# Performance work log

Measured on AMD Instinct MI355X. Metric: run time of the kernel, lower is better.

## Reference

```python
import jax, jax.numpy as jnp
import numpy as np

# ---- static config (matches init_kwargs) ----
N, E = 8192, 262144
IN_CH, MP_CH, HID, K = 128, 512, 256, 10
EPS, DELTA = 1e-3, 0.311
TV_COEFF, BAL_COEFF = 0.785, 0.514


def setup_inputs() -> dict:
    key = jax.random.key(0)
    ks = jax.random.split(key, 16)

    def p(k, shape):
        fan_in = shape[0] if len(shape) > 1 else shape[0]
        return (jax.random.normal(k, shape, jnp.float32) / np.sqrt(fan_in)).astype(jnp.float32)

    return {
        "x": jax.random.normal(ks[0], (N, IN_CH), jnp.float32),
        "edge_index": jax.random.randint(ks[1], (2, E), 0, N, jnp.int32),
        "edge_weight": jax.random.uniform(ks[2], (E,), jnp.float32),
        # GTVConv layer 1 / 2 (Linear weight + bias)
        "W1": p(ks[3], (IN_CH, MP_CH)), "b1": jnp.zeros((MP_CH,), jnp.float32),
        "W2": p(ks[4], (MP_CH, MP_CH)), "b2": jnp.zeros((MP_CH,), jnp.float32),
        # pooling MLP [512 -> 256 -> K], relu, no norm
        "Wm1": p(ks[5], (MP_CH, HID)), "bm1": jnp.zeros((HID,), jnp.float32),
        "Wm2": p(ks[6], (HID, K)), "bm2": jnp.zeros((K,), jnp.float32),
    }


def _gtv_conv(x, src, dst, w, W, b):
    """GTVConv: out = elu( h - delta*(D_G h - Gamma h) + b ),
    gamma_ij = w_ij / max(||h_i - h_j||_1, eps), h = x @ W."""
    h = x @ W                                   # [N, C]
    diff = jnp.sum(jnp.abs(h[src] - h[dst]), axis=-1)   # [E]
    gamma = w / jnp.maximum(diff, EPS)                  # [E]
    deg = jnp.zeros(h.shape[0], h.dtype).at[dst].add(gamma)          # [N]
    agg = jnp.zeros_like(h).at[dst].add(gamma[:, None] * h[src])     # Gamma @ h
    out = h - DELTA * (deg[:, None] * h - agg) + b
    return jax.nn.elu(out)


def reference(x, edge_index, edge_weight, W1, b1, W2, b2, Wm1, bm1, Wm2, bm2):
    src, dst = edge_index[0], edge_index[1]

    h = _gtv_conv(x, src, dst, edge_weight, W1, b1)
    h = _gtv_conv(h, src, dst, edge_weight, W2, b2)

    # pooling MLP -> cluster logits s
    s_logits = jax.nn.relu(h @ Wm1 + bm1) @ Wm2 + bm2   # [N, K]

    # dense adjacency (to_dense_adj: duplicate edges accumulate)
    adj = jnp.zeros((N, N), x.dtype).at[src, dst].add(edge_weight)

    s = jax.nn.softmax(s_logits, axis=-1)

    # total-variation loss: sum_ij a_ij * sum_k |s_ik - s_jk| / (2 * nnz(adj))
    tv = jnp.zeros((), x.dtype)
    for k in range(K):  # small fixed loop over clusters, avoids [N,N,K] tensor
        col = s[:, k]
        tv = tv + jnp.sum(adj * jnp.abs(col[:, None] - col[None, :]))
    n_edges = jax.lax.stop_gradient(jnp.count_nonzero(adj).astype(x.dtype))
    tv = tv / (2.0 * n_edges)

    # asymmetric-norm balance loss (AsymCheegerCut)
    idx = N // K + 1                         # rho-quantile index (static)
    quant = jnp.sort(s, axis=0)[N - idx]     # idx-th largest per cluster, [K]
    t = s - quant[None, :]
    asym = jnp.where(t >= 0, (K - 1) * t, -t)
    denom = float(N * (K - 1))
    bal = (denom - jnp.sum(asym)) / denom

    return s_logits, TV_COEFF * tv, BAL_COEFF * bal
```

## Files before the change

### kernel.cpp

```cpp
#include <hip/hip_runtime.h>

#define N_NODES 8192
#define N_EDGES 262144
#define IN_CH 128
#define MP_CH 512
#define HID 256
#define KCL 10
#define EPS_C 0.001f
#define DELTA_C 0.311f
#define TV_COEFF_C 0.785f
#define BAL_COEFF_C 0.514f
#define RANK1 7373
#define DBINS 80

typedef __bf16 bf16x8 __attribute__((ext_vector_type(8)));
typedef float f32x4 __attribute__((ext_vector_type(4)));
typedef unsigned short ushort8 __attribute__((ext_vector_type(8)));

__device__ __forceinline__ float bf2f(unsigned short h) {
  union { unsigned int u; float f; } c; c.u = ((unsigned int)h) << 16; return c.f;
}
__device__ __forceinline__ unsigned short f2bf(float f) {
  union { float f; unsigned int u; } c; c.f = f;
  unsigned int r = c.u + 0x7fffu + ((c.u >> 16) & 1u);
  return (unsigned short)(r >> 16);
}

__global__ void prep_kernel(const float* __restrict__ x, const float* __restrict__ W1,
                            const float* __restrict__ W2, const float* __restrict__ Wm1,
                            unsigned short* __restrict__ xb, unsigned short* __restrict__ W1bt,
                            unsigned short* __restrict__ W2bt, unsigned short* __restrict__ Wm1bt,
                            const int* __restrict__ dst, int* __restrict__ cnt) {
  int i = blockIdx.x * 256 + threadIdx.x;
  if (i < 1048576) { xb[i] = f2bf(x[i]); return; }
  i -= 1048576;
  if (i < 65536) { int n = i >> 7, k = i & 127; W1bt[i] = f2bf(W1[k * MP_CH + n]); return; }
  i -= 65536;
  if (i < 262144) { int n = i >> 9, k = i & 511; W2bt[i] = f2bf(W2[k * MP_CH + n]); return; }
  i -= 262144;
  if (i < 131072) { int n = i >> 9, k = i & 511; Wm1bt[i] = f2bf(Wm1[k * HID + n]); return; }
  i -= 131072;
  if (i < N_EDGES) atomicAdd(&cnt[dst[i]], 1);
}

__global__ __launch_bounds__(1024) void scan_kernel(const int* __restrict__ cnt,
                                                    int* __restrict__ offs,
                                                    int* __restrict__ cursor,
                                                    int* __restrict__ nodeorder) {
  __shared__ int ts[1024];
  __shared__ int dh[DBINS];
  int t = threadIdx.x;
  int v[8]; int s = 0;
#pragma unroll
  for (int j = 0; j < 8; ++j) { v[j] = cnt[t * 8 + j]; s += v[j]; }
  if (t < DBINS) dh[t] = 0;
  ts[t] = s; __syncthreads();
  for (int off = 1; off < 1024; off <<= 1) {
    int add = (t >= off) ? ts[t - off] : 0;
    __syncthreads();
    ts[t] += add;
    __syncthreads();
  }
  int base = ts[t] - s;
#pragma unroll
  for (int j = 0; j < 8; ++j) {
    offs[t * 8 + j] = base; cursor[t * 8 + j] = base; base += v[j];
    int key = v[j] < (DBINS - 1) ? v[j] : (DBINS - 1);
    atomicAdd(&dh[(DBINS - 1) - key], 1);
  }
  if (t == 1023) offs[N_NODES] = ts[1023];
  __syncthreads();
  if (t == 0) {
    int acc0 = 0;
    for (int b = 0; b < DBINS; ++b) { int c = dh[b]; dh[b] = acc0; acc0 += c; }
  }
  __syncthreads();
#pragma unroll
  for (int j = 0; j < 8; ++j) {
    int key = v[j] < (DBINS - 1) ? v[j] : (DBINS - 1);
    int pos = atomicAdd(&dh[(DBINS - 1) - key], 1);
    nodeorder[pos] = t * 8 + j;
  }
}

__global__ void fill_kernel(const int* __restrict__ src, const int* __restrict__ dst,
                            const float* __restrict__ ew, int* __restrict__ cursor,
                            int2* __restrict__ esw) {
  for (int e = blockIdx.x * blockDim.x + threadIdx.x; e < N_EDGES; e += gridDim.x * blockDim.x) {
    int p = atomicAdd(&cursor[dst[e]], 1);
    esw[p] = make_int2(src[e], __float_as_int(ew[e]));
  }
}

__global__ __launch_bounds__(256) void gemm_bt(
    const unsigned short* __restrict__ A, const unsigned short* __restrict__ BT,
    float* __restrict__ C, unsigned short* __restrict__ Cb,
    const float* __restrict__ bias, int N, int K, int epi) {
  __shared__ unsigned short lsm[2 * 128 * 32];
  unsigned short* lA = lsm;
  unsigned short* lB = lsm + 128 * 32;
  int lane = threadIdx.x & 63;
  int wv = threadIdx.x >> 6;
  int tm = blockIdx.y * 128, tn = blockIdx.x * 128;
  int wm = (wv >> 1) * 64, wn = (wv & 1) * 64;
  int rA = lane & 15, quad = lane >> 4;
  f32x4 acc[4][4];
#pragma unroll
  for (int i = 0; i < 4; ++i)
#pragma unroll
    for (int j = 0; j < 4; ++j) acc[i][j] = (f32x4){0.f, 0.f, 0.f, 0.f};

  int arow = wv * 32 + (lane >> 2);
  int acol = (lane & 3) * 8;

  for (int k0 = 0; k0 < K; k0 += 32) {
#pragma unroll
    for (int c = 0; c < 2; ++c) {
      const unsigned short* ga = A + (size_t)(tm + arow + c * 16) * K + k0 + acol;
      __builtin_amdgcn_global_load_lds(
          (const __attribute__((address_space(1))) unsigned int*)ga,
          (__attribute__((address_space(3))) unsigned int*)(lA + (wv * 32 + c * 16) * 32),
          16, 0, 0);
      const unsigned short* gb = BT + (size_t)(tn + arow + c * 16) * K + k0 + acol;
      __builtin_amdgcn_global_load_lds(
          (const __attribute__((address_space(1))) unsigned int*)gb,
          (__attribute__((address_space(3))) unsigned int*)(lB + (wv * 32 + c * 16) * 32),
          16, 0, 0);
    }
    __syncthreads();
    bf16x8 af[4], bfr[4];
#pragma unroll
    for (int i = 0; i < 4; ++i)
      af[i] = *(const bf16x8*)(lA + (wm + i * 16 + rA) * 32 + quad * 8);
#pragma unroll
    for (int j = 0; j < 4; ++j)
      bfr[j] = *(const bf16x8*)(lB + (wn + j * 16 + rA) * 32 + quad * 8);
#pragma unroll
    for (int i = 0; i < 4; ++i)
#pragma unroll
      for (int j = 0; j < 4; ++j)
        acc[i][j] = __builtin_amdgcn_mfma_f32_16x16x32_bf16(af[i], bfr[j], acc[i][j], 0, 0, 0);
    __syncthreads();
  }

  if (epi == 1) {
#pragma unroll
    for (int i = 0; i < 4; ++i)
#pragma unroll
      for (int j = 0; j < 4; ++j)
#pragma unroll
        for (int r = 0; r < 4; ++r) {
          int row = tm + wm + i * 16 + quad * 4 + r;
          int col = tn + wn + j * 16 + rA;
          float v = acc[i][j][r] + bias[col];
          C[(size_t)row * N + col] = fmaxf(v, 0.f);
        }
  } else {
    float* fbuf = (float*)lsm;
    int band = threadIdx.x >> 7;
    int rrow = (threadIdx.x >> 3) & 15;
    int cg = threadIdx.x & 7;
#pragma unroll
    for (int i = 0; i < 4; ++i) {
#pragma unroll
      for (int j = 0; j < 4; ++j)
#pragma unroll
        for (int r = 0; r < 4; ++r)
          fbuf[(wv >> 1) * (16 * 128) + (quad * 4 + r) * 128 + (wn + j * 16 + rA)] =
              acc[i][j][r];
      __syncthreads();
      const float* sr = fbuf + band * (16 * 128) + rrow * 128 + cg * 16;
      unsigned short ov[16];
#pragma unroll
      for (int c = 0; c < 16; ++c) ov[c] = f2bf(sr[c]);
      size_t base = (size_t)(tm + band * 64 + i * 16 + rrow) * N + tn + cg * 16;
      *(ushort8*)(Cb + base) = *(ushort8*)ov;
      *(ushort8*)(Cb + base + 8) = *(ushort8*)(ov + 8);
      __syncthreads();
    }
  }
}

__global__ __launch_bounds__(256, 8) void gtv_node(
    const unsigned short* __restrict__ hb, const float* __restrict__ bias,
    const int2* __restrict__ esw, const int* __restrict__ offs,
    const int* __restrict__ nodeorder, unsigned short* __restrict__ outb) {
  __shared__ float sacc[2][MP_CH];
  int lane = threadIdx.x & 63;
  int wv = threadIdx.x >> 6;
  int pair = wv >> 1;
  int half = wv & 1;
  int d = __builtin_amdgcn_readfirstlane(nodeorder[blockIdx.x * 2 + pair]);
  ushort8 hdv = ((const ushort8*)(hb + (size_t)d * MP_CH))[lane];
  float hd[8], acc[8];
#pragma unroll
  for (int j = 0; j < 8; ++j) { hd[j] = bf2f(hdv[j]); acc[j] = 0.f; }
  int n0 = offs[d], n1 = offs[d + 1];
  int mid = n0 + ((n1 - n0 + 1) >> 1);
  int e0 = half ? mid : n0;
  int e1 = half ? n1 : mid;
  int i = e0;
  for (; i + 1 < e1; i += 2) {
    int2 ma = esw[i], mb = esw[i + 1];
    float wa = __int_as_float(ma.y), wb = __int_as_float(mb.y);
    ushort8 va = ((const ushort8*)(hb + (size_t)ma.x * MP_CH))[lane];
    ushort8 vb = ((const ushort8*)(hb + (size_t)mb.x * MP_CH))[lane];
    float pa = 0.f, pb = 0.f;
#pragma unroll
    for (int j = 0; j < 8; ++j) {
      pa += fabsf(hd[j] - bf2f(va[j]));
      pb += fabsf(hd[j] - bf2f(vb[j]));
    }
#pragma unroll
    for (int m = 1; m < 64; m <<= 1) { pa += __shfl_xor(pa, m, 64); pb += __shfl_xor(pb, m, 64); }
    float ga = wa * __builtin_amdgcn_rcpf(fmaxf(pa, EPS_C));
    float gb = wb * __builtin_amdgcn_rcpf(fmaxf(pb, EPS_C));
#pragma unroll
    for (int j = 0; j < 8; ++j)
      acc[j] += ga * (hd[j] - bf2f(va[j])) + gb * (hd[j] - bf2f(vb[j]));
  }
  if (i < e1) {
    int2 m0 = esw[i];
    float w = __int_as_float(m0.y);
    ushort8 sv = ((const ushort8*)(hb + (size_t)m0.x * MP_CH))[lane];
    float part = 0.f;
#pragma unroll
    for (int j = 0; j < 8; ++j) part += fabsf(hd[j] - bf2f(sv[j]));
#pragma unroll
    for (int m = 1; m < 64; m <<= 1) part += __shfl_xor(part, m, 64);
    float g = w * __builtin_amdgcn_rcpf(fmaxf(part, EPS_C));
#pragma unroll
    for (int j = 0; j < 8; ++j) acc[j] += g * (hd[j] - bf2f(sv[j]));
  }
  if (half) {
#pragma unroll
    for (int j = 0; j < 8; ++j) sacc[pair][lane * 8 + j] = acc[j];
  }
  __syncthreads();
  if (!half) {
    const f32x4* br = (const f32x4*)(bias + lane * 8);
    f32x4 b0 = br[0], b1 = br[1];
    unsigned short ov[8];
#pragma unroll
    for (int j = 0; j < 8; ++j) {
      float tot = acc[j] + sacc[pair][lane * 8 + j];
      float bv = (j < 4) ? b0[j] : b1[j - 4];
      float o = hd[j] - DELTA_C * tot + bv;
      o = (o > 0.f) ? o : (expf(o) - 1.f);
      ov[j] = f2bf(o);
    }
    *((ushort8*)(outb + (size_t)d * MP_CH) + lane) = *(ushort8*)ov;
  }
}

__global__ __launch_bounds__(256) void gemm_small(
    const float* __restrict__ hm, const float* __restrict__ W,
    const float* __restrict__ b, float* __restrict__ out, float* __restrict__ s) {
  __shared__ float lw[HID * KCL];
  __shared__ float lb[KCL];
  for (int i = threadIdx.x; i < HID * KCL; i += 256) lw[i] = W[i];
  if (threadIdx.x < KCL) lb[threadIdx.x] = b[threadIdx.x];
  __syncthreads();
  int lane = threadIdx.x & 63, wv = threadIdx.x >> 6;
  int row = blockIdx.x * 4 + wv;
  f32x4 hv = *(const f32x4*)(hm + (size_t)row * HID + lane * 4);
  float p[KCL];
#pragma unroll
  for (int n = 0; n < KCL; ++n) {
    int k0 = lane * 4;
    p[n] = hv[0] * lw[(k0 + 0) * KCL + n] + hv[1] * lw[(k0 + 1) * KCL + n] +
           hv[2] * lw[(k0 + 2) * KCL + n] + hv[3] * lw[(k0 + 3) * KCL + n];
  }
#pragma unroll
  for (int n = 0; n < KCL; ++n)
#pragma unroll
    for (int m = 1; m < 64; m <<= 1) p[n] += __shfl_xor(p[n], m, 64);
  if (lane == 0) {
    float vv[KCL]; float mx = -1e30f;
#pragma unroll
    for (int n = 0; n < KCL; ++n) {
      vv[n] = p[n] + lb[n];
      out[(size_t)row * KCL + n] = vv[n];
      mx = fmaxf(mx, vv[n]);
    }
    float sum = 0.f;
#pragma unroll
    for (int n = 0; n < KCL; ++n) { vv[n] = expf(vv[n] - mx); sum += vv[n]; }
    float inv = 1.f / sum;
#pragma unroll
    for (int n = 0; n < KCL; ++n) s[(size_t)row * KCL + n] = vv[n] * inv;
  }
}

__global__ __launch_bounds__(1024) void tvquant_kernel(
    const int* __restrict__ src, const int* __restrict__ dst,
    const float* __restrict__ ew, const float* __restrict__ s,
    unsigned int* __restrict__ bitmap, float* __restrict__ scal) {
  __shared__ float fsh[16];
  __shared__ int wcnt[2][16];
  int t = threadIdx.x;
  int lane = t & 63, wv = t >> 6;
  if (blockIdx.x < 246) {
    float local = 0.f;
    for (int e = blockIdx.x * 1024 + t; e < N_EDGES; e += 246 * 1024) {
      int a = src[e], b = dst[e];
      float w = ew[e];
      const float* sa = s + (size_t)a * KCL;
      const float* sb = s + (size_t)b * KCL;
      float tv = 0.f;
#pragma unroll
      for (int k = 0; k < KCL; ++k) tv += fabsf(sa[k] - sb[k]);
      local += w * tv;
      if (w != 0.f) {
        unsigned int key = ((unsigned int)a << 13) | (unsigned int)b;
        atomicOr(&bitmap[key >> 5], 1u << (key & 31u));
      }
    }
#pragma unroll
    for (int m = 1; m < 64; m <<= 1) local += __shfl_xor(local, m, 64);
    if (lane == 0) fsh[wv] = local;
    __syncthreads();
    if (t == 0) {
      float tot = 0.f;
#pragma unroll
      for (int i2 = 0; i2 < 16; ++i2) tot += fsh[i2];
      atomicAdd(&scal[0], tot);
    }
  } else {
    int k = blockIdx.x - 246;
    unsigned int v[8];
#pragma unroll
    for (int j = 0; j < 8; ++j)
      v[j] = __float_as_uint(s[(size_t)(t + j * 1024) * KCL + k]);
    unsigned int lo = 0u, hi = 0x3F800000u;
    int p = 0;
    while (lo < hi) {
      unsigned int mid = (lo + hi) >> 1;
      int c = 0;
#pragma unroll
      for (int j = 0; j < 8; ++j) c += (v[j] <= mid) ? 1 : 0;
#pragma unroll
      for (int m = 1; m < 64; m <<= 1) c += __shfl_xor(c, m, 64);
      if (lane == 0) wcnt[p][wv] = c;
      __syncthreads();
      int tot = 0;
#pragma unroll
      for (int i2 = 0; i2 < 16; ++i2) tot += wcnt[p][i2];
      if (tot >= RANK1) hi = mid; else lo = mid + 1;
      p ^= 1;
    }
    float q = __uint_as_float(lo);
    float local = 0.f;
#pragma unroll
    for (int j = 0; j < 8; ++j) {
      float tt = __uint_as_float(v[j]) - q;
      local += (tt >= 0.f) ? 9.f * tt : -tt;
    }
#pragma unroll
    for (int m = 1; m < 64; m <<= 1) local += __shfl_xor(local, m, 64);
    if (lane == 0) fsh[wv] = local;
    __syncthreads();
    if (t == 0) {
      float tot = 0.f;
#pragma unroll
      for (int i2 = 0; i2 < 16; ++i2) tot += fsh[i2];
      atomicAdd(&scal[1], tot);
    }
  }
}

__global__ __launch_bounds__(1024) void popcfin_kernel(const unsigned int* __restrict__ bm,
                                                       float* __restrict__ scal,
                                                       float* __restrict__ out) {
  __shared__ int ish[16];
  int t = threadIdx.x;
  int lane = t & 63, wv = t >> 6;
  int local = 0;
  for (int i = blockIdx.x * 1024 + t; i < (1 << 21); i += 256 * 1024)
    local += __popc(bm[i]);
#pragma unroll
  for (int m = 1; m < 64; m <<= 1) local += __shfl_xor(local, m, 64);
  if (lane == 0) ish[wv] = local;
  __syncthreads();
  if (t == 0) {
    int tot = 0;
#pragma unroll
    for (int i2 = 0; i2 < 16; ++i2) tot += ish[i2];
    atomicAdd((int*)(scal + 2), tot);
    __threadfence();
    int d = atomicAdd((int*)(scal + 3), 1);
    if (d == 255) {
      float tv = scal[0], asym = scal[1];
      float nedges = (float)(*(int*)(scal + 2));
      out[N_NODES * KCL] = TV_COEFF_C * (tv / (2.f * nedges));
      out[N_NODES * KCL + 1] = BAL_COEFF_C * ((73728.f - asym) / 73728.f);
    }
  }
}

#define OFF_BM     ((size_t)0)
#define OFF_CNT    ((size_t)8388608)
#define OFF_SCAL   ((size_t)8421376)
#define OFF_OFFS   ((size_t)8421888)
#define OFF_CURSOR ((size_t)8454912)
#define OFF_NORD   ((size_t)8487936)
#define OFF_HB     ((size_t)16777216)
#define OFF_OUTB   ((size_t)25165824)
#define OFF_HM     ((size_t)33554432)
#define OFF_XB     ((size_t)41943040)
#define OFF_W1BT   ((size_t)44040192)
#define OFF_W2BT   ((size_t)44171264)
#define OFF_WM1BT  ((size_t)44695552)
#define OFF_S      ((size_t)44957696)

extern "C" void kernel_launch(void* const* d_in, const int* in_sizes, int n_in,
                              void* d_out, int out_size, void* d_ws, size_t ws_size,
                              hipStream_t stream) {
  const float* x   = (const float*)d_in[0];
  const int*   ei  = (const int*)d_in[1];
  const float* ew  = (const float*)d_in[2];
  const float* W1  = (const float*)d_in[3];
  const float* b1  = (const float*)d_in[4];
  const float* W2  = (const float*)d_in[5];
  const float* b2  = (const float*)d_in[6];
  const float* Wm1 = (const float*)d_in[7];
  const float* bm1 = (const float*)d_in[8];
  const float* Wm2 = (const float*)d_in[9];
  const float* bm2 = (const float*)d_in[10];
  float* out = (float*)d_out;

  char* ws = (char*)d_ws;
  unsigned int*   bitmap = (unsigned int*)(ws + OFF_BM);
  int*            cnt    = (int*)(ws + OFF_CNT);
  float*          scal   = (float*)(ws + OFF_SCAL);
  int*            offs   = (int*)(ws + OFF_OFFS);
  int*            cursor = (int*)(ws + OFF_CURSOR);
  int*            nord   = (int*)(ws + OFF_NORD);
  unsigned short* hb     = (unsigned short*)(ws + OFF_HB);
  unsigned short* outb   = (unsigned short*)(ws + OFF_OUTB);
  float*          hm     = (float*)(ws + OFF_HM);
  int2*           esw    = (int2*)(ws + OFF_HM);
  unsigned short* xb     = (unsigned short*)(ws + OFF_XB);
  unsigned short* W1bt   = (unsigned short*)(ws + OFF_W1BT);
  unsigned short* W2bt   = (unsigned short*)(ws + OFF_W2BT);
  unsigned short* Wm1bt  = (unsigned short*)(ws + OFF_WM1BT);
  float*          s      = (float*)(ws + OFF_S);

  const int* srcA = ei;
  const int* dstA = ei + N_EDGES;

  hipMemsetAsync(ws, 0, 8421632, stream);

  prep_kernel<<<6912, 256, 0, stream>>>(x, W1, W2, Wm1, xb, W1bt, W2bt, Wm1bt, dstA, cnt);
  scan_kernel<<<1, 1024, 0, stream>>>(cnt, offs, cursor, nord);
  fill_kernel<<<1024, 256, 0, stream>>>(srcA, dstA, ew, cursor, esw);

  gemm_bt<<<dim3(MP_CH / 128, N_NODES / 128), 256, 0, stream>>>(
      xb, W1bt, nullptr, hb, nullptr, MP_CH, IN_CH, 2);
  gtv_node<<<N_NODES / 2, 256, 0, stream>>>(hb, b1, esw, offs, nord, outb);
  gemm_bt<<<dim3(MP_CH / 128, N_NODES / 128), 256, 0, stream>>>(
      outb, W2bt, nullptr, hb, nullptr, MP_CH, MP_CH, 2);
  gtv_node<<<N_NODES / 2, 256, 0, stream>>>(hb, b2, esw, offs, nord, outb);
  gemm_bt<<<dim3(HID / 128, N_NODES / 128), 256, 0, stream>>>(
      outb, Wm1bt, hm, nullptr, bm1, HID, MP_CH, 1);
  gemm_small<<<N_NODES / 4, 256, 0, stream>>>(hm, Wm2, bm2, out, s);

  tvquant_kernel<<<256, 1024, 0, stream>>>(srcA, dstA, ew, s, bitmap, scal);
  popcfin_kernel<<<256, 1024, 0, stream>>>(bitmap, scal, out);
}
```

Measured before the change: 259.4 us.

## Switch intermediate storage from bf16 to fp16 and use packed half math in GTV aggregation

```diff
diff --git a/kernel.cpp b/kernel.cpp
--- a/kernel.cpp
+++ b/kernel.cpp
@@ -13,32 +13,32 @@
 #define RANK1 7373
 #define DBINS 80
 
-typedef __bf16 bf16x8 __attribute__((ext_vector_type(8)));
+typedef _Float16 f16x8 __attribute__((ext_vector_type(8)));
+typedef _Float16 f16x2 __attribute__((ext_vector_type(2)));
 typedef float f32x4 __attribute__((ext_vector_type(4)));
-typedef unsigned short ushort8 __attribute__((ext_vector_type(8)));
-
-__device__ __forceinline__ float bf2f(unsigned short h) {
-  union { unsigned int u; float f; } c; c.u = ((unsigned int)h) << 16; return c.f;
-}
-__device__ __forceinline__ unsigned short f2bf(float f) {
-  union { float f; unsigned int u; } c; c.f = f;
-  unsigned int r = c.u + 0x7fffu + ((c.u >> 16) & 1u);
-  return (unsigned short)(r >> 16);
+
+__device__ __forceinline__ f16x2 habs2(f16x2 a) {
+  unsigned int u;
+  __builtin_memcpy(&u, &a, 4);
+  u &= 0x7FFF7FFFu;
+  f16x2 r;
+  __builtin_memcpy(&r, &u, 4);
+  return r;
 }
 
 __global__ void prep_kernel(const float* __restrict__ x, const float* __restrict__ W1,
                             const float* __restrict__ W2, const float* __restrict__ Wm1,
-                            unsigned short* __restrict__ xb, unsigned short* __restrict__ W1bt,
-                            unsigned short* __restrict__ W2bt, unsigned short* __restrict__ Wm1bt,
+                            _Float16* __restrict__ xb, _Float16* __restrict__ W1bt,
+                            _Float16* __restrict__ W2bt, _Float16* __restrict__ Wm1bt,
                             const int* __restrict__ dst, int* __restrict__ cnt) {
   int i = blockIdx.x * 256 + threadIdx.x;
-  if (i < 1048576) { xb[i] = f2bf(x[i]); return; }
+  if (i < 1048576) { xb[i] = (_Float16)x[i]; return; }
   i -= 1048576;
-  if (i < 65536) { int n = i >> 7, k = i & 127; W1bt[i] = f2bf(W1[k * MP_CH + n]); return; }
+  if (i < 65536) { int n = i >> 7, k = i & 127; W1bt[i] = (_Float16)W1[k * MP_CH + n]; return; }
   i -= 65536;
-  if (i < 262144) { int n = i >> 9, k = i & 511; W2bt[i] = f2bf(W2[k * MP_CH + n]); return; }
+  if (i < 262144) { int n = i >> 9, k = i & 511; W2bt[i] = (_Float16)W2[k * MP_CH + n]; return; }
   i -= 262144;
-  if (i < 131072) { int n = i >> 9, k = i & 511; Wm1bt[i] = f2bf(Wm1[k * HID + n]); return; }
+  if (i < 131072) { int n = i >> 9, k = i & 511; Wm1bt[i] = (_Float16)Wm1[k * HID + n]; return; }
   i -= 131072;
   if (i < N_EDGES) atomicAdd(&cnt[dst[i]], 1);
 }
@@ -93,12 +93,12 @@
 }
 
 __global__ __launch_bounds__(256) void gemm_bt(
-    const unsigned short* __restrict__ A, const unsigned short* __restrict__ BT,
-    float* __restrict__ C, unsigned short* __restrict__ Cb,
+    const _Float16* __restrict__ A, const _Float16* __restrict__ BT,
+    float* __restrict__ C, _Float16* __restrict__ Cb,
     const float* __restrict__ bias, int N, int K, int epi) {
-  __shared__ unsigned short lsm[2 * 128 * 32];
-  unsigned short* lA = lsm;
-  unsigned short* lB = lsm + 128 * 32;
+  __shared__ _Float16 lsm[2 * 128 * 32];
+  _Float16* lA = lsm;
+  _Float16* lB = lsm + 128 * 32;
   int lane = threadIdx.x & 63;
   int wv = threadIdx.x >> 6;
   int tm = blockIdx.y * 128, tn = blockIdx.x * 128;
@@ -116,30 +116,30 @@
   for (int k0 = 0; k0 < K; k0 += 32) {
 #pragma unroll
     for (int c = 0; c < 2; ++c) {
-      const unsigned short* ga = A + (size_t)(tm + arow + c * 16) * K + k0 + acol;
+      const _Float16* ga = A + (size_t)(tm + arow + c * 16) * K + k0 + acol;
       __builtin_amdgcn_global_load_lds(
           (const __attribute__((address_space(1))) unsigned int*)ga,
           (__attribute__((address_space(3))) unsigned int*)(lA + (wv * 32 + c * 16) * 32),
           16, 0, 0);
-      const unsigned short* gb = BT + (size_t)(tn + arow + c * 16) * K + k0 + acol;
+      const _Float16* gb = BT + (size_t)(tn + arow + c * 16) * K + k0 + acol;
       __builtin_amdgcn_global_load_lds(
           (const __attribute__((address_space(1))) unsigned int*)gb,
           (__attribute__((address_space(3))) unsigned int*)(lB + (wv * 32 + c * 16) * 32),
           16, 0, 0);
     }
     __syncthreads();
-    bf16x8 af[4], bfr[4];
+    f16x8 af[4], bfr[4];
 #pragma unroll
     for (int i = 0; i < 4; ++i)
-      af[i] = *(const bf16x8*)(lA + (wm + i * 16 + rA) * 32 + quad * 8);
+      af[i] = *(const f16x8*)(lA + (wm + i * 16 + rA) * 32 + quad * 8);
 #pragma unroll
     for (int j = 0; j < 4; ++j)
-      bfr[j] = *(const bf16x8*)(lB + (wn + j * 16 + rA) * 32 + quad * 8);
+      bfr[j] = *(const f16x8*)(lB + (wn + j * 16 + rA) * 32 + quad * 8);
 #pragma unroll
     for (int i = 0; i < 4; ++i)
 #pragma unroll
       for (int j = 0; j < 4; ++j)
-        acc[i][j] = __builtin_amdgcn_mfma_f32_16x16x32_bf16(af[i], bfr[j], acc[i][j], 0, 0, 0);
+        acc[i][j] = __builtin_amdgcn_mfma_f32_16x16x32_f16(af[i], bfr[j], acc[i][j], 0, 0, 0);
     __syncthreads();
   }
 
@@ -170,31 +170,35 @@
               acc[i][j][r];
       __syncthreads();
       const float* sr = fbuf + band * (16 * 128) + rrow * 128 + cg * 16;
-      unsigned short ov[16];
-#pragma unroll
-      for (int c = 0; c < 16; ++c) ov[c] = f2bf(sr[c]);
+      f16x8 o1, o2;
+#pragma unroll
+      for (int c = 0; c < 8; ++c) { o1[c] = (_Float16)sr[c]; o2[c] = (_Float16)sr[c + 8]; }
       size_t base = (size_t)(tm + band * 64 + i * 16 + rrow) * N + tn + cg * 16;
-      *(ushort8*)(Cb + base) = *(ushort8*)ov;
-      *(ushort8*)(Cb + base + 8) = *(ushort8*)(ov + 8);
+      *(f16x8*)(Cb + base) = o1;
+      *(f16x8*)(Cb + base + 8) = o2;
       __syncthreads();
     }
   }
 }
 
 __global__ __launch_bounds__(256, 8) void gtv_node(
-    const unsigned short* __restrict__ hb, const float* __restrict__ bias,
+    const _Float16* __restrict__ hb, const float* __restrict__ bias,
     const int2* __restrict__ esw, const int* __restrict__ offs,
-    const int* __restrict__ nodeorder, unsigned short* __restrict__ outb) {
+    const int* __restrict__ nodeorder, _Float16* __restrict__ outb) {
   __shared__ float sacc[2][MP_CH];
+  const f16x2 one2 = {(_Float16)1.0f, (_Float16)1.0f};
   int lane = threadIdx.x & 63;
   int wv = threadIdx.x >> 6;
   int pair = wv >> 1;
   int half = wv & 1;
   int d = __builtin_amdgcn_readfirstlane(nodeorder[blockIdx.x * 2 + pair]);
-  ushort8 hdv = ((const ushort8*)(hb + (size_t)d * MP_CH))[lane];
-  float hd[8], acc[8];
-#pragma unroll
-  for (int j = 0; j < 8; ++j) { hd[j] = bf2f(hdv[j]); acc[j] = 0.f; }
+  f16x8 hdv = ((const f16x8*)(hb + (size_t)d * MP_CH))[lane];
+  f16x2 hd2[4], acc2[4];
+#pragma unroll
+  for (int p = 0; p < 4; ++p) {
+    hd2[p] = (f16x2){hdv[2 * p], hdv[2 * p + 1]};
+    acc2[p] = (f16x2){(_Float16)0.f, (_Float16)0.f};
+  }
   int n0 = offs[d], n1 = offs[d + 1];
   int mid = n0 + ((n1 - n0 + 1) >> 1);
   int e0 = half ? mid : n0;
@@ -203,53 +207,71 @@
   for (; i + 1 < e1; i += 2) {
     int2 ma = esw[i], mb = esw[i + 1];
     float wa = __int_as_float(ma.y), wb = __int_as_float(mb.y);
-    ushort8 va = ((const ushort8*)(hb + (size_t)ma.x * MP_CH))[lane];
-    ushort8 vb = ((const ushort8*)(hb + (size_t)mb.x * MP_CH))[lane];
+    f16x8 va = ((const f16x8*)(hb + (size_t)ma.x * MP_CH))[lane];
+    f16x8 vb = ((const f16x8*)(hb + (size_t)mb.x * MP_CH))[lane];
+    f16x2 da[4], db[4];
     float pa = 0.f, pb = 0.f;
 #pragma unroll
-    for (int j = 0; j < 8; ++j) {
-      pa += fabsf(hd[j] - bf2f(va[j]));
-      pb += fabsf(hd[j] - bf2f(vb[j]));
+    for (int p = 0; p < 4; ++p) {
+      f16x2 av = (f16x2){va[2 * p], va[2 * p + 1]};
+      f16x2 bv = (f16x2){vb[2 * p], vb[2 * p + 1]};
+      da[p] = hd2[p] - av;
+      db[p] = hd2[p] - bv;
+      pa = __builtin_amdgcn_fdot2(habs2(da[p]), one2, pa, false);
+      pb = __builtin_amdgcn_fdot2(habs2(db[p]), one2, pb, false);
     }
 #pragma unroll
     for (int m = 1; m < 64; m <<= 1) { pa += __shfl_xor(pa, m, 64); pb += __shfl_xor(pb, m, 64); }
     float ga = wa * __builtin_amdgcn_rcpf(fmaxf(pa, EPS_C));
     float gb = wb * __builtin_amdgcn_rcpf(fmaxf(pb, EPS_C));
-#pragma unroll
-    for (int j = 0; j < 8; ++j)
-      acc[j] += ga * (hd[j] - bf2f(va[j])) + gb * (hd[j] - bf2f(vb[j]));
+    f16x2 ga2 = {(_Float16)ga, (_Float16)ga};
+    f16x2 gb2 = {(_Float16)gb, (_Float16)gb};
+#pragma unroll
+    for (int p = 0; p < 4; ++p) {
+      acc2[p] += ga2 * da[p];
+      acc2[p] += gb2 * db[p];
+    }
   }
   if (i < e1) {
     int2 m0 = esw[i];
     float w = __int_as_float(m0.y);
-    ushort8 sv = ((const ushort8*)(hb + (size_t)m0.x * MP_CH))[lane];
+    f16x8 sv = ((const f16x8*)(hb + (size_t)m0.x * MP_CH))[lane];
+    f16x2 ds[4];
     float part = 0.f;
 #pragma unroll
-    for (int j = 0; j < 8; ++j) part += fabsf(hd[j] - bf2f(sv[j]));
+    for (int p = 0; p < 4; ++p) {
+      f16x2 svp = (f16x2){sv[2 * p], sv[2 * p + 1]};
+      ds[p] = hd2[p] - svp;
+      part = __builtin_amdgcn_fdot2(habs2(ds[p]), one2, part, false);
+    }
 #pragma unroll
     for (int m = 1; m < 64; m <<= 1) part += __shfl_xor(part, m, 64);
     float g = w * __builtin_amdgcn_rcpf(fmaxf(part, EPS_C));
-#pragma unroll
-    for (int j = 0; j < 8; ++j) acc[j] += g * (hd[j] - bf2f(sv[j]));
+    f16x2 g2 = {(_Float16)g, (_Float16)g};
+#pragma unroll
+    for (int p = 0; p < 4; ++p) acc2[p] += g2 * ds[p];
   }
   if (half) {
 #pragma unroll
-    for (int j = 0; j < 8; ++j) sacc[pair][lane * 8 + j] = acc[j];
+    for (int p = 0; p < 4; ++p) {
+      sacc[pair][lane * 8 + 2 * p] = (float)acc2[p][0];
+      sacc[pair][lane * 8 + 2 * p + 1] = (float)acc2[p][1];
+    }
   }
   __syncthreads();
   if (!half) {
     const f32x4* br = (const f32x4*)(bias + lane * 8);
     f32x4 b0 = br[0], b1 = br[1];
-    unsigned short ov[8];
+    f16x8 ov;
 #pragma unroll
     for (int j = 0; j < 8; ++j) {
-      float tot = acc[j] + sacc[pair][lane * 8 + j];
+      float aj = (float)acc2[j >> 1][j & 1] + sacc[pair][lane * 8 + j];
       float bv = (j < 4) ? b0[j] : b1[j - 4];
-      float o = hd[j] - DELTA_C * tot + bv;
+      float o = (float)hdv[j] - DELTA_C * aj + bv;
       o = (o > 0.f) ? o : (expf(o) - 1.f);
-      ov[j] = f2bf(o);
-    }
-    *((ushort8*)(outb + (size_t)d * MP_CH) + lane) = *(ushort8*)ov;
+      ov[j] = (_Float16)o;
+    }
+    ((f16x8*)(outb + (size_t)d * MP_CH))[lane] = ov;
   }
 }
 
@@ -430,21 +452,21 @@
   float* out = (float*)d_out;
 
   char* ws = (char*)d_ws;
-  unsigned int*   bitmap = (unsigned int*)(ws + OFF_BM);
-  int*            cnt    = (int*)(ws + OFF_CNT);
-  float*          scal   = (float*)(ws + OFF_SCAL);
-  int*            offs   = (int*)(ws + OFF_OFFS);
-  int*            cursor = (int*)(ws + OFF_CURSOR);
-  int*            nord   = (int*)(ws + OFF_NORD);
-  unsigned short* hb     = (unsigned short*)(ws + OFF_HB);
-  unsigned short* outb   = (unsigned short*)(ws + OFF_OUTB);
-  float*          hm     = (float*)(ws + OFF_HM);
-  int2*           esw    = (int2*)(ws + OFF_HM);
-  unsigned short* xb     = (unsigned short*)(ws + OFF_XB);
-  unsigned short* W1bt   = (unsigned short*)(ws + OFF_W1BT);
-  unsigned short* W2bt   = (unsigned short*)(ws + OFF_W2BT);
-  unsigned short* Wm1bt  = (unsigned short*)(ws + OFF_WM1BT);
-  float*          s      = (float*)(ws + OFF_S);
+  unsigned int* bitmap = (unsigned int*)(ws + OFF_BM);
+  int*          cnt    = (int*)(ws + OFF_CNT);
+  float*        scal   = (float*)(ws + OFF_SCAL);
+  int*          offs   = (int*)(ws + OFF_OFFS);
+  int*          cursor = (int*)(ws + OFF_CURSOR);
+  int*          nord   = (int*)(ws + OFF_NORD);
+  _Float16*     hb     = (_Float16*)(ws + OFF_HB);
+  _Float16*     outb   = (_Float16*)(ws + OFF_OUTB);
+  float*        hm     = (float*)(ws + OFF_HM);
+  int2*         esw    = (int2*)(ws + OFF_HM);
+  _Float16*     xb     = (_Float16*)(ws + OFF_XB);
+  _Float16*     W1bt   = (_Float16*)(ws + OFF_W1BT);
+  _Float16*     W2bt   = (_Float16*)(ws + OFF_W2BT);
+  _Float16*     Wm1bt  = (_Float16*)(ws + OFF_WM1BT);
+  float*        s      = (float*)(ws + OFF_S);
 
   const int* srcA = ei;
   const int* dstA = ei + N_EDGES;
```

Result: slower. 265.8 us (+2.5%).

## Count unique edges via CSR dedup instead of dense bitmap and popcount

Applied to the files above, without the earlier changes.

```diff
diff --git a/kernel.cpp b/kernel.cpp
--- a/kernel.cpp
+++ b/kernel.cpp
@@ -92,6 +92,29 @@
   }
 }
 
+__global__ __launch_bounds__(256) void dedup_kernel(const int2* __restrict__ esw,
+                                                    const int* __restrict__ offs,
+                                                    float* __restrict__ scal) {
+  __shared__ int wsum[4];
+  int lane = threadIdx.x & 63;
+  int wv = threadIdx.x >> 6;
+  int d = blockIdx.x * 4 + wv;
+  int e0 = offs[d], e1 = offs[d + 1];
+  int cnt = 0;
+  for (int p = e0 + lane; p < e1; p += 64) {
+    int sp = esw[p].x;
+    bool dup = false;
+    for (int q = e0; q < p; ++q) dup |= (esw[q].x == sp);
+    cnt += dup ? 0 : 1;
+  }
+#pragma unroll
+  for (int m = 1; m < 64; m <<= 1) cnt += __shfl_xor(cnt, m, 64);
+  if (lane == 0) wsum[wv] = cnt;
+  __syncthreads();
+  if (threadIdx.x == 0)
+    atomicAdd((int*)(scal + 2), wsum[0] + wsum[1] + wsum[2] + wsum[3]);
+}
+
 __global__ __launch_bounds__(256) void gemm_bt(
     const unsigned short* __restrict__ A, const unsigned short* __restrict__ BT,
     float* __restrict__ C, unsigned short* __restrict__ Cb,
@@ -295,7 +318,7 @@
 __global__ __launch_bounds__(1024) void tvquant_kernel(
     const int* __restrict__ src, const int* __restrict__ dst,
     const float* __restrict__ ew, const float* __restrict__ s,
-    unsigned int* __restrict__ bitmap, float* __restrict__ scal) {
+    float* __restrict__ scal, float* __restrict__ out) {
   __shared__ float fsh[16];
   __shared__ int wcnt[2][16];
   int t = threadIdx.x;
@@ -311,10 +334,6 @@
 #pragma unroll
       for (int k = 0; k < KCL; ++k) tv += fabsf(sa[k] - sb[k]);
       local += w * tv;
-      if (w != 0.f) {
-        unsigned int key = ((unsigned int)a << 13) | (unsigned int)b;
-        atomicOr(&bitmap[key >> 5], 1u << (key & 31u));
-      }
     }
 #pragma unroll
     for (int m = 1; m < 64; m <<= 1) local += __shfl_xor(local, m, 64);
@@ -367,29 +386,10 @@
       atomicAdd(&scal[1], tot);
     }
   }
-}
-
-__global__ __launch_bounds__(1024) void popcfin_kernel(const unsigned int* __restrict__ bm,
-                                                       float* __restrict__ scal,
-                                                       float* __restrict__ out) {
-  __shared__ int ish[16];
-  int t = threadIdx.x;
-  int lane = t & 63, wv = t >> 6;
-  int local = 0;
-  for (int i = blockIdx.x * 1024 + t; i < (1 << 21); i += 256 * 1024)
-    local += __popc(bm[i]);
-#pragma unroll
-  for (int m = 1; m < 64; m <<= 1) local += __shfl_xor(local, m, 64);
-  if (lane == 0) ish[wv] = local;
-  __syncthreads();
   if (t == 0) {
-    int tot = 0;
-#pragma unroll
-    for (int i2 = 0; i2 < 16; ++i2) tot += ish[i2];
-    atomicAdd((int*)(scal + 2), tot);
     __threadfence();
-    int d = atomicAdd((int*)(scal + 3), 1);
-    if (d == 255) {
+    int dn = atomicAdd((int*)(scal + 3), 1);
+    if (dn == 255) {
       float tv = scal[0], asym = scal[1];
       float nedges = (float)(*(int*)(scal + 2));
       out[N_NODES * KCL] = TV_COEFF_C * (tv / (2.f * nedges));
@@ -398,12 +398,11 @@
   }
 }
 
-#define OFF_BM     ((size_t)0)
-#define OFF_CNT    ((size_t)8388608)
-#define OFF_SCAL   ((size_t)8421376)
-#define OFF_OFFS   ((size_t)8421888)
-#define OFF_CURSOR ((size_t)8454912)
-#define OFF_NORD   ((size_t)8487936)
+#define OFF_CNT    ((size_t)0)
+#define OFF_SCAL   ((size_t)32768)
+#define OFF_OFFS   ((size_t)33280)
+#define OFF_CURSOR ((size_t)66560)
+#define OFF_NORD   ((size_t)99328)
 #define OFF_HB     ((size_t)16777216)
 #define OFF_OUTB   ((size_t)25165824)
 #define OFF_HM     ((size_t)33554432)
@@ -430,7 +429,6 @@
   float* out = (float*)d_out;
 
   char* ws = (char*)d_ws;
-  unsigned int*   bitmap = (unsigned int*)(ws + OFF_BM);
   int*            cnt    = (int*)(ws + OFF_CNT);
   float*          scal   = (float*)(ws + OFF_SCAL);
   int*            offs   = (int*)(ws + OFF_OFFS);
@@ -449,11 +447,12 @@
   const int* srcA = ei;
   const int* dstA = ei + N_EDGES;
 
-  hipMemsetAsync(ws, 0, 8421632, stream);
+  hipMemsetAsync(ws, 0, 33024, stream);
 
   prep_kernel<<<6912, 256, 0, stream>>>(x, W1, W2, Wm1, xb, W1bt, W2bt, Wm1bt, dstA, cnt);
   scan_kernel<<<1, 1024, 0, stream>>>(cnt, offs, cursor, nord);
   fill_kernel<<<1024, 256, 0, stream>>>(srcA, dstA, ew, cursor, esw);
+  dedup_kernel<<<N_NODES / 4, 256, 0, stream>>>(esw, offs, scal);
 
   gemm_bt<<<dim3(MP_CH / 128, N_NODES / 128), 256, 0, stream>>>(
       xb, W1bt, nullptr, hb, nullptr, MP_CH, IN_CH, 2);
@@ -465,6 +464,5 @@
       outb, Wm1bt, hm, nullptr, bm1, HID, MP_CH, 1);
   gemm_small<<<N_NODES / 4, 256, 0, stream>>>(hm, Wm2, bm2, out, s);
 
-  tvquant_kernel<<<256, 1024, 0, stream>>>(srcA, dstA, ew, s, bitmap, scal);
-  popcfin_kernel<<<256, 1024, 0, stream>>>(bitmap, scal, out);
-}
+  tvquant_kernel<<<256, 1024, 0, stream>>>(srcA, dstA, ew, s, scal, out);
+}
```

New measurement: 270.8 us. 1.04x slower.
